# Optimization experiments

Measured on AMD Instinct MI355X. Metric: run time of the kernel, lower is better.

## Reference

```python
import jax, jax.numpy as jnp
import numpy as np

E = 800000   # num edges
N = 50000    # num atoms
C = 128      # in_channels
RBF = 20     # rbf_dim
T = 1        # num_target


def setup_inputs() -> dict:
    key = jax.random.key(0)
    ks = jax.random.split(key, 12)
    return {
        "x_scalar": jax.random.normal(ks[0], (E, C), dtype=jnp.float32),
        "rbf": jax.random.normal(ks[1], (E, RBF), dtype=jnp.float32),
        "envelop_para": jax.random.uniform(ks[2], (E, 1), dtype=jnp.float32),
        "edge_index_0": jax.random.randint(ks[3], (E,), 0, N),
        "num_atoms": N,
        # learned parameters (biases initialized to zero per reset_parameters)
        "W_rbf": jax.random.normal(ks[4], (C, RBF), dtype=jnp.float32) * 0.05,
        "b_rbf": jnp.zeros((C,), dtype=jnp.float32),
        "W1": jax.random.normal(ks[5], (C, C), dtype=jnp.float32) * 0.05,
        "b1": jnp.zeros((C,), dtype=jnp.float32),
        "W2": jax.random.normal(ks[6], (C, C), dtype=jnp.float32) * 0.05,
        "b2": jnp.zeros((C,), dtype=jnp.float32),
        "W3": jax.random.normal(ks[7], (T, C), dtype=jnp.float32) * 0.05,
        "b3": jnp.zeros((T,), dtype=jnp.float32),
    }


def reference(x_scalar, rbf, envelop_para, edge_index_0, num_atoms,
              W_rbf, b_rbf, W1, b1, W2, b2, W3, b3):
    # per-edge filter: Linear(rbf) * envelope, then modulate node features
    rbf_filter = (rbf @ W_rbf.T + b_rbf) * envelop_para  # [E, C]
    msg = rbf_filter * x_scalar                           # [E, C]
    # scatter_add over destination atoms
    out = jax.ops.segment_sum(msg, edge_index_0, num_segments=num_atoms)  # [N, C]
    # small MLP head: Linear+SiLU, Linear+SiLU, Linear -> num_target
    out = jax.nn.silu(out @ W1.T + b1)
    out = jax.nn.silu(out @ W2.T + b2)
    out = out @ W3.T + b3                                 # [N, T]
    return out
```

## Files before the change

### kernel.cpp

```cpp
#include <hip/hip_runtime.h>
#include <hip/hip_bf16.h>

#define C 128
#define RBFD 20
#define NATOMS 50000
#define SCAN_CHUNK 1024
#define SLAB 64

__global__ __launch_bounds__(256) void setup_kernel(
    const float* __restrict__ W1, const float* __restrict__ W2,
    float* __restrict__ W1T, float* __restrict__ W2T,
    int* __restrict__ count, float4* __restrict__ acc4,
    int n, int acc_quads)
{
    const int t = blockIdx.x * blockDim.x + threadIdx.x;
    const int stride = gridDim.x * blockDim.x;
    if (t < C * C) {
        int k = t / C;
        int c = t % C;
        W1T[t] = W1[c * C + k];
        W2T[t] = W2[c * C + k];
    }
    for (int i = t; i < n; i += stride) count[i] = 0;
    const float4 z = make_float4(0.f, 0.f, 0.f, 0.f);
    for (int i = t; i < acc_quads; i += stride) acc4[i] = z;
}

__global__ __launch_bounds__(256) void histogram_kernel(
    const int* __restrict__ idx, int* __restrict__ count, int E)
{
    int e = blockIdx.x * blockDim.x + threadIdx.x;
    if (e < E) atomicAdd(&count[idx[e]], 1);
}

__global__ __launch_bounds__(256) void scan_partials_kernel(
    const int* __restrict__ count, int* __restrict__ partial, int n)
{
    __shared__ int sm[256];
    const int start = blockIdx.x * SCAN_CHUNK;
    int s = 0;
    for (int i = threadIdx.x; i < SCAN_CHUNK; i += 256) {
        int g = start + i;
        if (g < n) s += count[g];
    }
    sm[threadIdx.x] = s;
    __syncthreads();
    for (int off = 128; off > 0; off >>= 1) {
        if (threadIdx.x < off) sm[threadIdx.x] += sm[threadIdx.x + off];
        __syncthreads();
    }
    if (threadIdx.x == 0) partial[blockIdx.x] = sm[0];
}

__global__ void scan_chunkbase_kernel(int* __restrict__ partial,
                                      int* __restrict__ base,
                                      int nchunks, int n)
{
    if (threadIdx.x == 0 && blockIdx.x == 0) {
        int run = 0;
        for (int k = 0; k < nchunks; ++k) {
            int t = partial[k];
            partial[k] = run;
            run += t;
        }
        base[n] = run;
    }
}

__global__ __launch_bounds__(1024) void scan_apply_kernel(
    const int* __restrict__ count, const int* __restrict__ chunk_base,
    int* __restrict__ base, int* __restrict__ cursor, int n)
{
    __shared__ int sm[SCAN_CHUNK];
    const int t = threadIdx.x;
    const int i = blockIdx.x * SCAN_CHUNK + t;
    int v = (i < n) ? count[i] : 0;
    sm[t] = v;
    __syncthreads();
    for (int off = 1; off < SCAN_CHUNK; off <<= 1) {
        int tmp = (t >= off) ? sm[t - off] : 0;
        __syncthreads();
        sm[t] += tmp;
        __syncthreads();
    }
    if (i < n) {
        int excl = sm[t] - v + chunk_base[blockIdx.x];
        base[i] = excl;
        cursor[i] = excl;
    }
}

__global__ __launch_bounds__(256) void fill_perm_kernel(
    const int* __restrict__ idx, int* __restrict__ cursor,
    int* __restrict__ perm, int* __restrict__ own, int E)
{
    int e = blockIdx.x * blockDim.x + threadIdx.x;
    if (e < E) {
        int a = idx[e];
        int pos = atomicAdd(&cursor[a], 1);
        perm[pos] = e;
        own[pos] = a;
    }
}

struct R5 { float4 a, b, c, d, e; };

__device__ __forceinline__ R5 load_rbf5(const float* __restrict__ rbf, int eidx) {
    const float4* q = reinterpret_cast<const float4*>(rbf + (size_t)eidx * RBFD);
    R5 r;
    r.a = q[0]; r.b = q[1]; r.c = q[2]; r.d = q[3]; r.e = q[4];
    return r;
}

__device__ __forceinline__ float dot20(const R5& p, const float* __restrict__ w,
                                       float bias) {
    float f = bias;
    f = fmaf(p.a.x, w[0],  f); f = fmaf(p.a.y, w[1],  f);
    f = fmaf(p.a.z, w[2],  f); f = fmaf(p.a.w, w[3],  f);
    f = fmaf(p.b.x, w[4],  f); f = fmaf(p.b.y, w[5],  f);
    f = fmaf(p.b.z, w[6],  f); f = fmaf(p.b.w, w[7],  f);
    f = fmaf(p.c.x, w[8],  f); f = fmaf(p.c.y, w[9],  f);
    f = fmaf(p.c.z, w[10], f); f = fmaf(p.c.w, w[11], f);
    f = fmaf(p.d.x, w[12], f); f = fmaf(p.d.y, w[13], f);
    f = fmaf(p.d.z, w[14], f); f = fmaf(p.d.w, w[15], f);
    f = fmaf(p.e.x, w[16], f); f = fmaf(p.e.y, w[17], f);
    f = fmaf(p.e.z, w[18], f); f = fmaf(p.e.w, w[19], f);
    return f;
}

__global__ __launch_bounds__(64, 3) void gather_kernel(
    const float* __restrict__ x,
    const float* __restrict__ rbf,
    const float* __restrict__ env,
    const int*   __restrict__ perm,
    const int*   __restrict__ own,
    const float* __restrict__ Wrbf,
    const float* __restrict__ brbf,
    float* __restrict__ acc)
{
    __shared__ int  e_s[SLAB];
    __shared__ int2 oe_s[SLAB];

    const int tid  = threadIdx.x;
    const int bid  = blockIdx.x;
    const int slab = bid >> 1;
    const int ch   = ((bid & 1) << 6) | tid;
    const int p0   = slab << 6;

    {
        const int e = perm[p0 + tid];
        e_s[tid]  = e;
        oe_s[tid] = make_int2(own[p0 + tid], __float_as_int(env[e]));
    }

    float w[RBFD];
#pragma unroll
    for (int r = 0; r < RBFD; ++r) w[r] = Wrbf[ch * RBFD + r];
    const float bias = brbf[ch];

    __syncthreads();

    const int first_own = oe_s[0].x;
    int   cur_own = first_own;
    float sum = 0.0f;

#define FLUSH()                                                                \
    do {                                                                       \
        if (cur_own == first_own)                                              \
            unsafeAtomicAdd(&acc[(size_t)cur_own * C + ch], sum);              \
        else acc[(size_t)cur_own * C + ch] = sum;                              \
    } while (0)

    int   er[8];
    float xp[8];
#pragma unroll
    for (int i = 0; i < 8; ++i) {
        er[i] = e_s[i];
        xp[i] = x[((size_t)er[i] << 7) + ch];
    }
    R5 Pa = load_rbf5(rbf, er[0]);
    R5 Pb = load_rbf5(rbf, er[1]);
    __builtin_amdgcn_sched_barrier(0);

#pragma unroll
    for (int j = 0; j < SLAB; j += 2) {
        R5 Na, Nb;
        if (j + 2 < SLAB) {
            Na = load_rbf5(rbf, er[(j + 2) & 7]);
            Nb = load_rbf5(rbf, er[(j + 3) & 7]);
        }
        int en0 = 0, en1 = 0;
        float xn0 = 0.0f, xn1 = 0.0f;
        if (j + 8 < SLAB) { en0 = e_s[j + 8]; xn0 = x[((size_t)en0 << 7) + ch]; }
        if (j + 9 < SLAB) { en1 = e_s[j + 9]; xn1 = x[((size_t)en1 << 7) + ch]; }
        __builtin_amdgcn_sched_barrier(0);

        const int2 m0 = oe_s[j];
        const int2 m1 = oe_s[j + 1];
        const float f0 = dot20(Pa, w, bias);
        const float f1 = dot20(Pb, w, bias);
        const float v0 = f0 * __int_as_float(m0.y) * xp[j & 7];
        const float v1 = f1 * __int_as_float(m1.y) * xp[(j + 1) & 7];

        if (m0.x != cur_own) { FLUSH(); sum = 0.0f; cur_own = m0.x; }
        sum += v0;
        if (m1.x != cur_own) { FLUSH(); sum = 0.0f; cur_own = m1.x; }
        sum += v1;

        if (j + 8 < SLAB) { er[j & 7] = en0; xp[j & 7] = xn0; }
        if (j + 9 < SLAB) { er[(j + 1) & 7] = en1; xp[(j + 1) & 7] = xn1; }
        Pa = Na; Pb = Nb;
    }
    unsafeAtomicAdd(&acc[(size_t)cur_own * C + ch], sum);
#undef FLUSH
}

__device__ __forceinline__ float silu_f(float v) {
    return v * (1.0f / (1.0f + __expf(-v)));
}

__global__ __launch_bounds__(256) void mlp_head_kernel(
    const float* __restrict__ acc,
    const float* __restrict__ W1T,
    const float* __restrict__ b1,
    const float* __restrict__ W2T,
    const float* __restrict__ b2,
    const float* __restrict__ W3,
    const float* __restrict__ b3,
    float* __restrict__ out,
    int natoms)
{
    __shared__ float As[C][C + 1];

    const int tid = threadIdx.x;
    const int a0  = blockIdx.x * C;
    const int tc  = tid & 15;
    const int ta  = tid >> 4;
    const int abase = ta * 8;
    const int cbase = tc * 8;

    {
        const int sub = tid >> 7;
        const int k   = tid & 127;
        for (int pair = 0; pair < 64; ++pair) {
            const int al = pair * 2 + sub;
            const int a  = a0 + al;
            float v = (a < natoms) ? acc[(size_t)a * C + k] : 0.0f;
            As[k][al] = v;
        }
    }
    __syncthreads();

    float r[8][8];

#pragma unroll
    for (int i = 0; i < 8; ++i)
#pragma unroll
        for (int j = 0; j < 8; ++j) r[i][j] = 0.0f;

#pragma unroll 2
    for (int k = 0; k < C; ++k) {
        float4 bq0 = *reinterpret_cast<const float4*>(W1T + k * C + cbase);
        float4 bq1 = *reinterpret_cast<const float4*>(W1T + k * C + cbase + 4);
        float bv[8] = {bq0.x, bq0.y, bq0.z, bq0.w, bq1.x, bq1.y, bq1.z, bq1.w};
        float av[8];
#pragma unroll
        for (int i = 0; i < 8; ++i) av[i] = As[k][abase + i];
#pragma unroll
        for (int i = 0; i < 8; ++i)
#pragma unroll
            for (int j = 0; j < 8; ++j) r[i][j] = fmaf(av[i], bv[j], r[i][j]);
    }

    __syncthreads();
    {
        float bb[8];
#pragma unroll
        for (int j = 0; j < 8; ++j) bb[j] = b1[cbase + j];
#pragma unroll
        for (int i = 0; i < 8; ++i)
#pragma unroll
            for (int j = 0; j < 8; ++j)
                As[cbase + j][abase + i] = silu_f(r[i][j] + bb[j]);
    }
    __syncthreads();

#pragma unroll
    for (int i = 0; i < 8; ++i)
#pragma unroll
        for (int j = 0; j < 8; ++j) r[i][j] = 0.0f;

#pragma unroll 2
    for (int k = 0; k < C; ++k) {
        float4 bq0 = *reinterpret_cast<const float4*>(W2T + k * C + cbase);
        float4 bq1 = *reinterpret_cast<const float4*>(W2T + k * C + cbase + 4);
        float bv[8] = {bq0.x, bq0.y, bq0.z, bq0.w, bq1.x, bq1.y, bq1.z, bq1.w};
        float av[8];
#pragma unroll
        for (int i = 0; i < 8; ++i) av[i] = As[k][abase + i];
#pragma unroll
        for (int i = 0; i < 8; ++i)
#pragma unroll
            for (int j = 0; j < 8; ++j) r[i][j] = fmaf(av[i], bv[j], r[i][j]);
    }

    __syncthreads();

    {
        float bb[8], w3v[8];
#pragma unroll
        for (int j = 0; j < 8; ++j) bb[j] = b2[cbase + j];
        float4 wq0 = *reinterpret_cast<const float4*>(W3 + cbase);
        float4 wq1 = *reinterpret_cast<const float4*>(W3 + cbase + 4);
        w3v[0]=wq0.x; w3v[1]=wq0.y; w3v[2]=wq0.z; w3v[3]=wq0.w;
        w3v[4]=wq1.x; w3v[5]=wq1.y; w3v[6]=wq1.z; w3v[7]=wq1.w;

#pragma unroll
        for (int i = 0; i < 8; ++i) {
            float p = 0.0f;
#pragma unroll
            for (int j = 0; j < 8; ++j)
                p = fmaf(silu_f(r[i][j] + bb[j]), w3v[j], p);
            As[abase + i][tc] = p;
        }
    }
    __syncthreads();

    if (tid < C) {
        const int a = a0 + tid;
        if (a < natoms) {
            float s = 0.0f;
#pragma unroll
            for (int t = 0; t < 16; ++t) s += As[tid][t];
            out[a] = s + b3[0];
        }
    }
}

extern "C" void kernel_launch(void* const* d_in, const int* in_sizes, int n_in,
                              void* d_out, int out_size, void* d_ws, size_t ws_size,
                              hipStream_t stream) {
    const float* x      = (const float*)d_in[0];
    const float* rbf    = (const float*)d_in[1];
    const float* env    = (const float*)d_in[2];
    const int*   idx    = (const int*)  d_in[3];
    const float* Wrbf   = (const float*)d_in[5];
    const float* brbf   = (const float*)d_in[6];
    const float* W1     = (const float*)d_in[7];
    const float* b1     = (const float*)d_in[8];
    const float* W2     = (const float*)d_in[9];
    const float* b2     = (const float*)d_in[10];
    const float* W3     = (const float*)d_in[11];
    const float* b3     = (const float*)d_in[12];
    float*       out    = (float*)d_out;

    const int E = in_sizes[0] / C;
    const int N = NATOMS;
    const int nchunks = (N + SCAN_CHUNK - 1) / SCAN_CHUNK;

    float* acc     = (float*)d_ws;
    float* W1T     = acc + (size_t)N * C;
    float* W2T     = W1T + C * C;
    int*   count   = (int*)(W2T + C * C);
    int*   base    = count + N;
    int*   cursor  = base + (N + 1);
    int*   partial = cursor + N;
    int*   perm    = partial + 64;
    int*   own     = perm + E;

    setup_kernel<<<2048, 256, 0, stream>>>(W1, W2, W1T, W2T, count,
                                           (float4*)acc, N, (N * C) / 4);

    histogram_kernel<<<(E + 255) / 256, 256, 0, stream>>>(idx, count, E);
    scan_partials_kernel<<<nchunks, 256, 0, stream>>>(count, partial, N);
    scan_chunkbase_kernel<<<1, 64, 0, stream>>>(partial, base, nchunks, N);
    scan_apply_kernel<<<nchunks, SCAN_CHUNK, 0, stream>>>(count, partial, base, cursor, N);
    fill_perm_kernel<<<(E + 255) / 256, 256, 0, stream>>>(idx, cursor, perm, own, E);

    gather_kernel<<<(E / SLAB) * 2, 64, 0, stream>>>(x, rbf, env, perm, own,
                                                     Wrbf, brbf, acc);

    const int tiles = (N + C - 1) / C;
    mlp_head_kernel<<<tiles, 256, 0, stream>>>(acc, W1T, b1, W2T, b2, W3, b3, out, N);
}
```

Before: 367.5 us.

## Deepen gather prefetch to eight edges with inline-asm loads and vmcnt waits

Rewrites the gather kernel's inner loop as an 8-deep software pipeline. Each edge's rbf row and x element are issued with inline global_load instructions into a rotating register ring, and a manual s_waitcnt vmcnt keeps about seven edges of loads in flight. Occupancy in launch_bounds drops from 3 to 2 waves to make room for the extra registers. The aim is to hide gather memory latency through more memory-level parallelism per wave. The risk is that manual waitcnt counting depends on exact load counts, and the last iterations issue wrapped-around loads that do redundant work.

```diff
diff --git a/kernel.cpp b/kernel.cpp
--- a/kernel.cpp
+++ b/kernel.cpp
@@ -6,6 +6,7 @@
 #define NATOMS 50000
 #define SCAN_CHUNK 1024
 #define SLAB 64
+#define PD 8
 
 __global__ __launch_bounds__(256) void setup_kernel(
     const float* __restrict__ W1, const float* __restrict__ W2,
@@ -105,12 +106,24 @@
 
 struct R5 { float4 a, b, c, d, e; };
 
-__device__ __forceinline__ R5 load_rbf5(const float* __restrict__ rbf, int eidx) {
-    const float4* q = reinterpret_cast<const float4*>(rbf + (size_t)eidx * RBFD);
-    R5 r;
-    r.a = q[0]; r.b = q[1]; r.c = q[2]; r.d = q[3]; r.e = q[4];
-    return r;
-}
+#define GL_BATCH(slot, eidx)                                                   \
+    do {                                                                       \
+        const int e_ = (eidx);                                                 \
+        const float* rp_ = rbf + (size_t)e_ * RBFD;                            \
+        const float* xq_ = x + ((size_t)e_ << 7) + ch;                         \
+        asm volatile("global_load_dwordx4 %0, %1, off"                         \
+                     : "=v"(pr[slot].a) : "v"(rp_));                           \
+        asm volatile("global_load_dwordx4 %0, %1, off offset:16"               \
+                     : "=v"(pr[slot].b) : "v"(rp_));                           \
+        asm volatile("global_load_dwordx4 %0, %1, off offset:32"               \
+                     : "=v"(pr[slot].c) : "v"(rp_));                           \
+        asm volatile("global_load_dwordx4 %0, %1, off offset:48"               \
+                     : "=v"(pr[slot].d) : "v"(rp_));                           \
+        asm volatile("global_load_dwordx4 %0, %1, off offset:64"               \
+                     : "=v"(pr[slot].e) : "v"(rp_));                           \
+        asm volatile("global_load_dword %0, %1, off"                           \
+                     : "=v"(px[slot]) : "v"(xq_));                             \
+    } while (0)
 
 __device__ __forceinline__ float dot20(const R5& p, const float* __restrict__ w,
                                        float bias) {
@@ -128,7 +141,7 @@
     return f;
 }
 
-__global__ __launch_bounds__(64, 3) void gather_kernel(
+__global__ __launch_bounds__(64, 2) void gather_kernel(
     const float* __restrict__ x,
     const float* __restrict__ rbf,
     const float* __restrict__ env,
@@ -160,6 +173,13 @@
 
     __syncthreads();
 
+    asm volatile("" ::
+        "v"(w[0]), "v"(w[1]), "v"(w[2]), "v"(w[3]), "v"(w[4]),
+        "v"(w[5]), "v"(w[6]), "v"(w[7]), "v"(w[8]), "v"(w[9]),
+        "v"(w[10]), "v"(w[11]), "v"(w[12]), "v"(w[13]), "v"(w[14]),
+        "v"(w[15]), "v"(w[16]), "v"(w[17]), "v"(w[18]), "v"(w[19]),
+        "v"(bias));
+
     const int first_own = oe_s[0].x;
     int   cur_own = first_own;
     float sum = 0.0f;
@@ -171,45 +191,28 @@
         else acc[(size_t)cur_own * C + ch] = sum;                              \
     } while (0)
 
-    int   er[8];
-    float xp[8];
-#pragma unroll
-    for (int i = 0; i < 8; ++i) {
-        er[i] = e_s[i];
-        xp[i] = x[((size_t)er[i] << 7) + ch];
-    }
-    R5 Pa = load_rbf5(rbf, er[0]);
-    R5 Pb = load_rbf5(rbf, er[1]);
-    __builtin_amdgcn_sched_barrier(0);
-
-#pragma unroll
-    for (int j = 0; j < SLAB; j += 2) {
-        R5 Na, Nb;
-        if (j + 2 < SLAB) {
-            Na = load_rbf5(rbf, er[(j + 2) & 7]);
-            Nb = load_rbf5(rbf, er[(j + 3) & 7]);
-        }
-        int en0 = 0, en1 = 0;
-        float xn0 = 0.0f, xn1 = 0.0f;
-        if (j + 8 < SLAB) { en0 = e_s[j + 8]; xn0 = x[((size_t)en0 << 7) + ch]; }
-        if (j + 9 < SLAB) { en1 = e_s[j + 9]; xn1 = x[((size_t)en1 << 7) + ch]; }
-        __builtin_amdgcn_sched_barrier(0);
-
-        const int2 m0 = oe_s[j];
-        const int2 m1 = oe_s[j + 1];
-        const float f0 = dot20(Pa, w, bias);
-        const float f1 = dot20(Pb, w, bias);
-        const float v0 = f0 * __int_as_float(m0.y) * xp[j & 7];
-        const float v1 = f1 * __int_as_float(m1.y) * xp[(j + 1) & 7];
-
-        if (m0.x != cur_own) { FLUSH(); sum = 0.0f; cur_own = m0.x; }
-        sum += v0;
-        if (m1.x != cur_own) { FLUSH(); sum = 0.0f; cur_own = m1.x; }
-        sum += v1;
-
-        if (j + 8 < SLAB) { er[j & 7] = en0; xp[j & 7] = xn0; }
-        if (j + 9 < SLAB) { er[(j + 1) & 7] = en1; xp[(j + 1) & 7] = xn1; }
-        Pa = Na; Pb = Nb;
+    R5    pr[PD];
+    float px[PD];
+
+#pragma unroll
+    for (int i = 0; i < PD; ++i) GL_BATCH(i, e_s[i]);
+
+#pragma unroll 1
+    for (int jo = 0; jo < SLAB; jo += PD) {
+#pragma unroll
+        for (int k = 0; k < PD; ++k) {
+            asm volatile("s_waitcnt vmcnt(42)" ::: "memory");
+            __builtin_amdgcn_sched_barrier(0);
+
+            const int2 m = oe_s[jo + k];
+            const float f = dot20(pr[k], w, bias);
+            const float v = f * __int_as_float(m.y) * px[k];
+
+            if (m.x != cur_own) { FLUSH(); sum = 0.0f; cur_own = m.x; }
+            sum += v;
+
+            GL_BATCH(k, e_s[(jo + k + PD) & (SLAB - 1)]);
+        }
     }
     unsafeAtomicAdd(&acc[(size_t)cur_own * C + ch], sum);
 #undef FLUSH
```

Measured after the change: 559.8 us. +52.3%, slower.
